# Kernel optimization log

Measured on AMD Instinct MI355X. Metric: run time of the kernel, lower is better.

Reference implementation:

```python
import jax, jax.numpy as jnp
import numpy as np

B, T, DIM = 2, 2048, 2048
N_HEADS, N_KV_HEADS = 32, 8
HEAD_DIM = DIM // N_HEADS          # 64
N_REP = N_HEADS // N_KV_HEADS      # 4
ROPE_THETA = 10000.0


def setup_inputs() -> dict:
    key = jax.random.key(0)
    ks = jax.random.split(key, 5)
    x = jax.random.normal(ks[0], (B, T, DIM), dtype=jnp.float32)
    # RoPE frequencies: freqs_cis[t, j] = exp(i * t * theta^{-2j/head_dim})
    inv_freq = 1.0 / (ROPE_THETA ** (jnp.arange(0, HEAD_DIM, 2, dtype=jnp.float32) / HEAD_DIM))
    angles = jnp.arange(T, dtype=jnp.float32)[:, None] * inv_freq[None, :]  # [T, HEAD_DIM//2]
    cos, sin = jnp.cos(angles), jnp.sin(angles)
    s = 0.02
    wq = jax.random.normal(ks[1], (N_HEADS * HEAD_DIM, DIM), dtype=jnp.float32) * s
    wk = jax.random.normal(ks[2], (N_KV_HEADS * HEAD_DIM, DIM), dtype=jnp.float32) * s
    wv = jax.random.normal(ks[3], (N_KV_HEADS * HEAD_DIM, DIM), dtype=jnp.float32) * s
    wo = jax.random.normal(ks[4], (DIM, DIM), dtype=jnp.float32) * s
    return {"x": x, "cos": cos, "sin": sin, "wq": wq, "wk": wk, "wv": wv, "wo": wo}


def _apply_rope(t, cos, sin):
    # t: [B, T, H, D]; cos/sin: [T, D//2]. Complex multiply on interleaved pairs.
    b, tt, h, d = t.shape
    tr = t.reshape(b, tt, h, d // 2, 2)
    t0, t1 = tr[..., 0], tr[..., 1]
    c = cos[None, :, None, :]
    s = sin[None, :, None, :]
    o0 = t0 * c - t1 * s
    o1 = t0 * s + t1 * c
    return jnp.stack([o0, o1], axis=-1).reshape(b, tt, h, d)


def reference(x, cos, sin, wq, wk, wv, wo):
    Bs, Ts, C = x.shape
    # Projections (nn.Linear, no bias): y = x @ W^T
    q = jnp.einsum('btc,oc->bto', x, wq).reshape(Bs, Ts, N_HEADS, HEAD_DIM)
    k = jnp.einsum('btc,oc->bto', x, wk).reshape(Bs, Ts, N_KV_HEADS, HEAD_DIM)
    v = jnp.einsum('btc,oc->bto', x, wv).reshape(Bs, Ts, N_KV_HEADS, HEAD_DIM)
    q = _apply_rope(q, cos[:Ts], sin[:Ts])
    k = _apply_rope(k, cos[:Ts], sin[:Ts])
    # [B, H, T, D]; GQA: broadcast kv heads via grouped einsum instead of repeat.
    q = q.transpose(0, 2, 1, 3).reshape(Bs, N_KV_HEADS, N_REP, Ts, HEAD_DIM)
    k = k.transpose(0, 2, 1, 3)  # [B, Hkv, T, D]
    v = v.transpose(0, 2, 1, 3)
    scale = 1.0 / jnp.sqrt(jnp.asarray(HEAD_DIM, dtype=x.dtype))
    scores = jnp.einsum('bgrqd,bgkd->bgrqk', q, k) * scale  # [B, Hkv, rep, T, T]
    causal = jnp.tril(jnp.ones((Ts, Ts), dtype=bool))
    scores = jnp.where(causal, scores, jnp.finfo(scores.dtype).min)
    attn = jax.nn.softmax(scores, axis=-1)
    y = jnp.einsum('bgrqk,bgkd->bgrqd', attn, v)           # [B, Hkv, rep, T, D]
    y = y.reshape(Bs, N_HEADS, Ts, HEAD_DIM).transpose(0, 2, 1, 3).reshape(Bs, Ts, C)
    return jnp.einsum('btc,oc->bto', y, wo)
```

## Files before the change

### kernel.cpp

```cpp
#include <hip/hip_runtime.h>

typedef __bf16 bf16;
typedef __attribute__((ext_vector_type(8))) __bf16 bf16x8;
typedef __attribute__((ext_vector_type(4))) __bf16 bf16x4;
typedef __attribute__((ext_vector_type(4))) float f32x4;

constexpr int T_SEQ = 2048;
constexpr int DIM   = 2048;
constexpr int NH    = 32;
constexpr int NKV   = 8;
constexpr int HD    = 64;
constexpr int QKV_N = DIM + 2 * NKV * HD;
constexpr int MROWS = 2 * T_SEQ;

__global__ void cast_all_kernel(const float* __restrict__ x,
                                const float* __restrict__ wq, const float* __restrict__ wk,
                                const float* __restrict__ wv, const float* __restrict__ wo,
                                bf16* __restrict__ xb, bf16* __restrict__ wqkv,
                                bf16* __restrict__ wob) {
  int stride = gridDim.x * blockDim.x;
  for (int g = blockIdx.x * blockDim.x + threadIdx.x; g < 4718592; g += stride) {
    const float* src; bf16* dst; int off;
    if (g < 2097152)      { src = x;  dst = xb;             off = g; }
    else if (g < 3145728) { src = wq; dst = wqkv;           off = g - 2097152; }
    else if (g < 3407872) { src = wk; dst = wqkv + 4194304; off = g - 3145728; }
    else if (g < 3670016) { src = wv; dst = wqkv + 5242880; off = g - 3407872; }
    else                  { src = wo; dst = wob;            off = g - 3670016; }
    float4 v = *(const float4*)(src + (size_t)off * 4);
    bf16x4 o = { (bf16)v.x, (bf16)v.y, (bf16)v.z, (bf16)v.w };
    *(bf16x4*)(dst + (size_t)off * 4) = o;
  }
}

template <typename OutT, bool ROPE>
__global__ __launch_bounds__(512) void gemm256(const bf16* __restrict__ A,
                                               const bf16* __restrict__ W,
                                               OutT* __restrict__ C,
                                               int N, int K, int cpx,
                                               const float* __restrict__ cs,
                                               const float* __restrict__ sn) {
  constexpr int BM = 256, BN = 128, BK = 64;
  __shared__ __attribute__((aligned(16))) bf16 Ab[3][BM * BK];
  __shared__ __attribute__((aligned(16))) bf16 Bb[3][BN * BK];
  const int tid = threadIdx.x, lane = tid & 63, wave = tid >> 6;
  const int l15 = lane & 15, l4 = lane >> 4;
  const int orig = blockIdx.x;
  const int wg = (orig & 7) * cpx + (orig >> 3);
  const int bm = (wg & 15) * BM;
  const int bn = (wg >> 4) * BN;
  const int wm = (wave >> 1) * 64, wn = (wave & 1) * 64;

  f32x4 acc[4][4] = {};

  const int NT = K / BK;
  auto stage = [&](int s, int k0) {
    #pragma unroll
    for (int i = 0; i < 4; ++i) {
      int c = i * 512 + tid;
      int row = c >> 3;
      int gc = ((c & 7) ^ (row & 7)) << 3;
      __builtin_amdgcn_global_load_lds(
          (const __attribute__((address_space(1))) unsigned int*)(A + (size_t)(bm + row) * K + k0 + gc),
          (__attribute__((address_space(3))) unsigned int*)(&Ab[s][0] + c * 8), 16, 0, 0);
    }
    #pragma unroll
    for (int i = 0; i < 2; ++i) {
      int c = i * 512 + tid;
      int row = c >> 3;
      int gc = ((c & 7) ^ (row & 7)) << 3;
      __builtin_amdgcn_global_load_lds(
          (const __attribute__((address_space(1))) unsigned int*)(W + (size_t)(bn + row) * K + k0 + gc),
          (__attribute__((address_space(3))) unsigned int*)(&Bb[s][0] + c * 8), 16, 0, 0);
    }
  };

  stage(0, 0);
  stage(1, BK);

  int d = 0;
  for (int t = 0; t < NT; ++t) {
    if (t + 1 < NT) { asm volatile("s_waitcnt vmcnt(6)" ::: "memory"); }
    else            { asm volatile("s_waitcnt vmcnt(0)" ::: "memory"); }
    __builtin_amdgcn_s_barrier();

    bf16x8 af[2][4], bfr[2][4];
    #pragma unroll
    for (int kk = 0; kk < 2; ++kk) {
      #pragma unroll
      for (int mi = 0; mi < 4; ++mi) {
        int row = wm + mi * 16 + l15;
        af[kk][mi] = *(const bf16x8*)((const char*)&Ab[d][0] + row * 128 +
                                      (((kk * 4 + l4) ^ (row & 7)) << 4));
      }
      #pragma unroll
      for (int ni = 0; ni < 4; ++ni) {
        int row = wn + ni * 16 + l15;
        bfr[kk][ni] = *(const bf16x8*)((const char*)&Bb[d][0] + row * 128 +
                                       (((kk * 4 + l4) ^ (row & 7)) << 4));
      }
    }

    if (t + 2 < NT) {
      int s = d + 2; if (s >= 3) s -= 3;
      stage(s, (t + 2) * BK);
    }

    __builtin_amdgcn_s_setprio(1);
    #pragma unroll
    for (int kk = 0; kk < 2; ++kk)
      #pragma unroll
      for (int mi = 0; mi < 4; ++mi)
        #pragma unroll
        for (int ni = 0; ni < 4; ++ni)
          acc[mi][ni] = __builtin_amdgcn_mfma_f32_16x16x32_bf16(af[kk][mi], bfr[kk][ni],
                                                                acc[mi][ni], 0, 0, 0);
    __builtin_amdgcn_s_setprio(0);

    ++d; if (d == 3) d = 0;
  }

  if constexpr (ROPE) {
    if (bn < 2560) {
      const bool odd = (l15 & 1);
      #pragma unroll
      for (int ni = 0; ni < 4; ++ni) {
        int col = bn + wn + ni * 16 + l15;
        int ip = (col & 63) >> 1;
        #pragma unroll
        for (int mi = 0; mi < 4; ++mi) {
          int row0 = wm + mi * 16 + l4 * 4;
          #pragma unroll
          for (int r = 0; r < 4; ++r) {
            int tpos = (bm + row0 + r) & (T_SEQ - 1);
            float c = cs[tpos * 32 + ip];
            float s = sn[tpos * 32 + ip];
            float a = acc[mi][ni][r];
            float p = __shfl_xor(a, 1);
            acc[mi][ni][r] = odd ? (p * s + a * c) : (a * c - p * s);
          }
        }
      }
    }
  }

  #pragma unroll
  for (int mi = 0; mi < 4; ++mi)
    #pragma unroll
    for (int ni = 0; ni < 4; ++ni) {
      size_t row = (size_t)bm + wm + mi * 16 + l4 * 4;
      int col = bn + wn + ni * 16 + l15;
      #pragma unroll
      for (int r = 0; r < 4; ++r)
        C[(row + r) * N + col] = (OutT)acc[mi][ni][r];
    }
}

__global__ __launch_bounds__(512, 2) void attn_kernel(const bf16* __restrict__ qkv,
                                                      bf16* __restrict__ y) {
  const int h = blockIdx.x, b = blockIdx.z;
  const int strip = 15 - blockIdx.y;
  const int g = h >> 2;
  const int tid = threadIdx.x, lane = tid & 63, wave = tid >> 6;
  const int l15 = lane & 15, l4 = lane >> 4;
  const int qbase = strip * 128 + wave * 16;

  __shared__ __attribute__((aligned(16))) bf16 Kb[2][128 * 64];
  __shared__ __attribute__((aligned(16))) bf16 VTs[2][2][64 * 64];
  __shared__ __attribute__((aligned(16))) bf16 Pb[8][16 * 64];

  constexpr float SCALE2 = 0.125f * 1.44269504088896f;
  constexpr float THR_RAW = 8.0f / SCALE2;
  constexpr int VOFF = DIM + NKV * HD;

  const bf16 one1 = (bf16)1.0f;
  const bf16x8 ones = { one1, one1, one1, one1, one1, one1, one1, one1 };

  bf16x8 qf[2];
  {
    const bf16* qp = qkv + ((size_t)b * T_SEQ + qbase + l15) * QKV_N + h * HD + l4 * 8;
    qf[0] = *(const bf16x8*)(qp);
    qf[1] = *(const bf16x8*)(qp + 32);
  }

  f32x4 oacc[4] = {};
  f32x4 lacc = {};
  float m_run = -INFINITY;
  const int qg = qbase + l15;

  const int nt = strip + 1;
  const size_t kvbase = (size_t)b * T_SEQ;
  const int vwoff = ((lane * 128 + wave * 16) ^ ((lane & 7) << 4));

  {
    #pragma unroll
    for (int i = 0; i < 2; ++i) {
      int chunk = i * 512 + tid;
      int row = chunk >> 3;
      int csrc = ((chunk & 7) << 3) ^ ((row & 7) << 3);
      __builtin_amdgcn_global_load_lds(
          (const __attribute__((address_space(1))) unsigned int*)
              (qkv + (kvbase + row) * QKV_N + DIM + g * HD + csrc),
          (__attribute__((address_space(3))) unsigned int*)(&Kb[0][0] + chunk * 8), 16, 0, 0);
    }
    #pragma unroll
    for (int hf = 0; hf < 2; ++hf) {
      const bf16* vp = qkv + (kvbase + hf * 64 + wave * 8) * QKV_N + VOFF + g * HD + lane;
      bf16x8 vr;
      #pragma unroll
      for (int j = 0; j < 8; ++j) vr[j] = vp[(size_t)j * QKV_N];
      *(bf16x8*)((char*)&VTs[0][hf][0] + vwoff) = vr;
    }
    asm volatile("s_waitcnt vmcnt(0)" ::: "memory");
    __syncthreads();
  }

  int cur = 0;
  for (int kt = 0; kt < nt; ++kt) {
    const bool has_next = (kt + 1) < nt;
    bf16x8 vr0, vr1;
    if (has_next) {
      #pragma unroll
      for (int i = 0; i < 2; ++i) {
        int chunk = i * 512 + tid;
        int row = chunk >> 3;
        int csrc = ((chunk & 7) << 3) ^ ((row & 7) << 3);
        __builtin_amdgcn_global_load_lds(
            (const __attribute__((address_space(1))) unsigned int*)
                (qkv + (kvbase + (kt + 1) * 128 + row) * QKV_N + DIM + g * HD + csrc),
            (__attribute__((address_space(3))) unsigned int*)(&Kb[cur ^ 1][0] + chunk * 8), 16, 0, 0);
      }
      const bf16* vp0 = qkv + (kvbase + (kt + 1) * 128 + wave * 8) * QKV_N + VOFF + g * HD + lane;
      const bf16* vp1 = vp0 + (size_t)64 * QKV_N;
      #pragma unroll
      for (int j = 0; j < 8; ++j) vr0[j] = vp0[(size_t)j * QKV_N];
      #pragma unroll
      for (int j = 0; j < 8; ++j) vr1[j] = vp1[(size_t)j * QKV_N];
    }

    const bf16* kb = &Kb[cur][0];
    const bool diag = (kt == strip);

    #pragma unroll
    for (int hf = 0; hf < 2; ++hf) {
      if (diag && hf == 1 && wave < 4) continue;

      f32x4 z[4];
      #pragma unroll
      for (int nt4 = 0; nt4 < 4; ++nt4) z[nt4] = (f32x4){0.f, 0.f, 0.f, 0.f};
      #pragma unroll
      for (int nt4 = 0; nt4 < 4; ++nt4)
        #pragma unroll
        for (int kk = 0; kk < 2; ++kk) {
          bf16x8 kf = *(const bf16x8*)((const char*)kb +
              (((hf * 64 + nt4 * 16 + l15) * 128 + (kk * 32 + l4 * 8) * 2) ^ ((l15 & 7) << 4)));
          z[nt4] = __builtin_amdgcn_mfma_f32_16x16x32_bf16(kf, qf[kk], z[nt4], 0, 0, 0);
        }

      if (diag) {
        #pragma unroll
        for (int nt4 = 0; nt4 < 4; ++nt4)
          #pragma unroll
          for (int r = 0; r < 4; ++r)
            if (kt * 128 + hf * 64 + nt4 * 16 + l4 * 4 + r > qg) z[nt4][r] = -INFINITY;
      }

      float a0 = fmaxf(fmaxf(z[0][0], z[0][1]), z[0][2]);
      float a1 = fmaxf(fmaxf(z[0][3], z[1][0]), z[1][1]);
      float a2 = fmaxf(fmaxf(z[1][2], z[1][3]), z[2][0]);
      float a3 = fmaxf(fmaxf(z[2][1], z[2][2]), z[2][3]);
      float a4 = fmaxf(fmaxf(z[3][0], z[3][1]), z[3][2]);
      float b0 = fmaxf(fmaxf(a0, a1), a2);
      float b1 = fmaxf(fmaxf(a3, a4), z[3][3]);
      float vm = fmaxf(b0, b1);
      vm = fmaxf(vm, __shfl_xor(vm, 16));
      vm = fmaxf(vm, __shfl_xor(vm, 32));

      if (!__all(vm - m_run <= THR_RAW)) {
        float mnew = fmaxf(m_run, vm);
        float alpha = __builtin_amdgcn_exp2f((m_run - mnew) * SCALE2);
        #pragma unroll
        for (int r = 0; r < 4; ++r) lacc[r] *= alpha;
        #pragma unroll
        for (int dt = 0; dt < 4; ++dt)
          #pragma unroll
          for (int r = 0; r < 4; ++r) oacc[dt][r] *= alpha;
        m_run = mnew;
      }
      const float ms = m_run * SCALE2;

      #pragma unroll
      for (int nt4 = 0; nt4 < 4; ++nt4)
        #pragma unroll
        for (int r = 0; r < 4; ++r)
          z[nt4][r] = __builtin_amdgcn_exp2f(__builtin_fmaf(z[nt4][r], SCALE2, -ms));

      bf16* pbw = &Pb[wave][0];
      #pragma unroll
      for (int nt4 = 0; nt4 < 4; ++nt4) {
        bf16x4 pk = { (bf16)z[nt4][0], (bf16)z[nt4][1], (bf16)z[nt4][2], (bf16)z[nt4][3] };
        *(bf16x4*)((char*)pbw + ((l15 * 128 + nt4 * 32 + l4 * 8) ^ ((l15 & 7) << 4))) = pk;
      }

      const bf16* vt = &VTs[cur][hf][0];
      #pragma unroll
      for (int kk = 0; kk < 2; ++kk) {
        bf16x8 pf = *(const bf16x8*)((const char*)pbw +
            ((l15 * 128 + kk * 64 + l4 * 16) ^ ((l15 & 7) << 4)));
        lacc = __builtin_amdgcn_mfma_f32_16x16x32_bf16(ones, pf, lacc, 0, 0, 0);
        #pragma unroll
        for (int dt = 0; dt < 4; ++dt) {
          bf16x8 vf = *(const bf16x8*)((const char*)vt +
              (((dt * 16 + l15) * 128 + (kk * 32 + l4 * 8) * 2) ^ ((l15 & 7) << 4)));
          oacc[dt] = __builtin_amdgcn_mfma_f32_16x16x32_bf16(vf, pf, oacc[dt], 0, 0, 0);
        }
      }
    }

    if (has_next) {
      *(bf16x8*)((char*)&VTs[cur ^ 1][0][0] + vwoff) = vr0;
      *(bf16x8*)((char*)&VTs[cur ^ 1][1][0] + vwoff) = vr1;
      __syncthreads();
      cur ^= 1;
    }
  }

  {
    float linv = __builtin_amdgcn_rcpf(lacc[0]);
    bf16* yp = y + ((size_t)b * T_SEQ + qbase + l15) * DIM + h * HD + l4 * 4;
    #pragma unroll
    for (int dt = 0; dt < 4; ++dt) {
      bf16x4 ov = { (bf16)(oacc[dt][0] * linv), (bf16)(oacc[dt][1] * linv),
                    (bf16)(oacc[dt][2] * linv), (bf16)(oacc[dt][3] * linv) };
      *(bf16x4*)(yp + dt * 16) = ov;
    }
  }
}

extern "C" void kernel_launch(void* const* d_in, const int* in_sizes, int n_in,
                              void* d_out, int out_size, void* d_ws, size_t ws_size,
                              hipStream_t stream) {
  const float* x    = (const float*)d_in[0];
  const float* cosb = (const float*)d_in[1];
  const float* sinb = (const float*)d_in[2];
  const float* wq   = (const float*)d_in[3];
  const float* wk   = (const float*)d_in[4];
  const float* wv   = (const float*)d_in[5];
  const float* wo   = (const float*)d_in[6];
  float* out = (float*)d_out;

  bf16* xb   = (bf16*)d_ws;
  bf16* wqkv = xb + (size_t)MROWS * DIM;
  bf16* wob  = wqkv + (size_t)QKV_N * DIM;
  bf16* qkv  = wob + (size_t)DIM * DIM;
  bf16* y    = qkv + (size_t)MROWS * QKV_N;

  cast_all_kernel<<<2048, 256, 0, stream>>>(x, wq, wk, wv, wo, xb, wqkv, wob);

  gemm256<bf16, true><<<384, 512, 0, stream>>>(xb, wqkv, qkv, QKV_N, DIM, 384 / 8, cosb, sinb);

  attn_kernel<<<dim3(NH, 16, 2), 512, 0, stream>>>(qkv, y);

  gemm256<float, false><<<256, 512, 0, stream>>>(y, wob, out, DIM, DIM, 256 / 8, nullptr, nullptr);
}
```

Measured before the change: 181.3 us.

## Use 256x192 tiles for QKV GEMM and rectangular block-to-tile mapping

New measurement: 164.4 us (median of 3 runs). 1.1x faster.

```diff
diff --git a/kernel.cpp b/kernel.cpp
--- a/kernel.cpp
+++ b/kernel.cpp
@@ -32,22 +32,24 @@
   }
 }
 
-template <typename OutT, bool ROPE>
+__device__ inline void rect_decode(int orig, int& bmi, int& bni) {
+  int c = orig & 7, i = orig >> 3;
+  bmi = (c & 1) * 8 + (i & 7);
+  bni = (c >> 1) * 4 + (i >> 3);
+}
+
 __global__ __launch_bounds__(512) void gemm256(const bf16* __restrict__ A,
                                                const bf16* __restrict__ W,
-                                               OutT* __restrict__ C,
-                                               int N, int K, int cpx,
-                                               const float* __restrict__ cs,
-                                               const float* __restrict__ sn) {
+                                               float* __restrict__ C,
+                                               int N, int K) {
   constexpr int BM = 256, BN = 128, BK = 64;
   __shared__ __attribute__((aligned(16))) bf16 Ab[3][BM * BK];
   __shared__ __attribute__((aligned(16))) bf16 Bb[3][BN * BK];
   const int tid = threadIdx.x, lane = tid & 63, wave = tid >> 6;
   const int l15 = lane & 15, l4 = lane >> 4;
-  const int orig = blockIdx.x;
-  const int wg = (orig & 7) * cpx + (orig >> 3);
-  const int bm = (wg & 15) * BM;
-  const int bn = (wg >> 4) * BN;
+  int bmi, bni;
+  rect_decode(blockIdx.x, bmi, bni);
+  const int bm = bmi * BM, bn = bni * BN;
   const int wm = (wave >> 1) * 64, wn = (wave & 1) * 64;
 
   f32x4 acc[4][4] = {};
@@ -119,30 +121,6 @@
     ++d; if (d == 3) d = 0;
   }
 
-  if constexpr (ROPE) {
-    if (bn < 2560) {
-      const bool odd = (l15 & 1);
-      #pragma unroll
-      for (int ni = 0; ni < 4; ++ni) {
-        int col = bn + wn + ni * 16 + l15;
-        int ip = (col & 63) >> 1;
-        #pragma unroll
-        for (int mi = 0; mi < 4; ++mi) {
-          int row0 = wm + mi * 16 + l4 * 4;
-          #pragma unroll
-          for (int r = 0; r < 4; ++r) {
-            int tpos = (bm + row0 + r) & (T_SEQ - 1);
-            float c = cs[tpos * 32 + ip];
-            float s = sn[tpos * 32 + ip];
-            float a = acc[mi][ni][r];
-            float p = __shfl_xor(a, 1);
-            acc[mi][ni][r] = odd ? (p * s + a * c) : (a * c - p * s);
-          }
-        }
-      }
-    }
-  }
-
   #pragma unroll
   for (int mi = 0; mi < 4; ++mi)
     #pragma unroll
@@ -151,7 +129,124 @@
       int col = bn + wn + ni * 16 + l15;
       #pragma unroll
       for (int r = 0; r < 4; ++r)
-        C[(row + r) * N + col] = (OutT)acc[mi][ni][r];
+        C[(row + r) * N + col] = acc[mi][ni][r];
+    }
+}
+
+__global__ __launch_bounds__(512, 1) void gemm192(const bf16* __restrict__ A,
+                                                  const bf16* __restrict__ W,
+                                                  bf16* __restrict__ C,
+                                                  const float* __restrict__ cs,
+                                                  const float* __restrict__ sn) {
+  constexpr int BM = 256, BN = 192, BK = 64, N = QKV_N, K = DIM;
+  __shared__ __attribute__((aligned(16))) bf16 Ab[3][BM * BK];
+  __shared__ __attribute__((aligned(16))) bf16 Bb[2][BN * BK];
+  const int tid = threadIdx.x, lane = tid & 63, wave = tid >> 6;
+  const int l15 = lane & 15, l4 = lane >> 4;
+  int bmi, bni;
+  rect_decode(blockIdx.x, bmi, bni);
+  const int bm = bmi * BM, bn = bni * BN;
+  const int wm = (wave >> 1) * 64, wn = (wave & 1) * 96;
+
+  f32x4 acc[4][6] = {};
+
+  constexpr int NT = K / BK;
+  auto stageA = [&](int s, int k0) {
+    #pragma unroll
+    for (int i = 0; i < 4; ++i) {
+      int c = i * 512 + tid;
+      int row = c >> 3;
+      int gc = ((c & 7) ^ (row & 7)) << 3;
+      __builtin_amdgcn_global_load_lds(
+          (const __attribute__((address_space(1))) unsigned int*)(A + (size_t)(bm + row) * K + k0 + gc),
+          (__attribute__((address_space(3))) unsigned int*)(&Ab[s][0] + c * 8), 16, 0, 0);
+    }
+  };
+  auto stageB = [&](int s, int k0) {
+    #pragma unroll
+    for (int i = 0; i < 3; ++i) {
+      int c = i * 512 + tid;
+      int row = c >> 3;
+      int gc = ((c & 7) ^ (row & 7)) << 3;
+      __builtin_amdgcn_global_load_lds(
+          (const __attribute__((address_space(1))) unsigned int*)(W + (size_t)(bn + row) * K + k0 + gc),
+          (__attribute__((address_space(3))) unsigned int*)(&Bb[s][0] + c * 8), 16, 0, 0);
+    }
+  };
+
+  stageA(0, 0);
+  stageB(0, 0);
+  stageA(1, BK);
+
+  for (int t = 0; t < NT; ++t) {
+    const int d3 = t % 3, db = t & 1;
+    if (t + 1 < NT) { asm volatile("s_waitcnt vmcnt(4)" ::: "memory"); }
+    else            { asm volatile("s_waitcnt vmcnt(0)" ::: "memory"); }
+    __builtin_amdgcn_s_barrier();
+
+    bf16x8 af[2][4], bfr[2][6];
+    #pragma unroll
+    for (int kk = 0; kk < 2; ++kk) {
+      #pragma unroll
+      for (int mi = 0; mi < 4; ++mi) {
+        int row = wm + mi * 16 + l15;
+        af[kk][mi] = *(const bf16x8*)((const char*)&Ab[d3][0] + row * 128 +
+                                      (((kk * 4 + l4) ^ (row & 7)) << 4));
+      }
+      #pragma unroll
+      for (int ni = 0; ni < 6; ++ni) {
+        int row = wn + ni * 16 + l15;
+        bfr[kk][ni] = *(const bf16x8*)((const char*)&Bb[db][0] + row * 128 +
+                                       (((kk * 4 + l4) ^ (row & 7)) << 4));
+      }
+    }
+
+    if (t + 1 < NT) stageB(db ^ 1, (t + 1) * BK);
+    if (t + 2 < NT) { int s = d3 + 2; if (s >= 3) s -= 3; stageA(s, (t + 2) * BK); }
+
+    __builtin_amdgcn_s_setprio(1);
+    #pragma unroll
+    for (int kk = 0; kk < 2; ++kk)
+      #pragma unroll
+      for (int mi = 0; mi < 4; ++mi)
+        #pragma unroll
+        for (int ni = 0; ni < 6; ++ni)
+          acc[mi][ni] = __builtin_amdgcn_mfma_f32_16x16x32_bf16(af[kk][mi], bfr[kk][ni],
+                                                                acc[mi][ni], 0, 0, 0);
+    __builtin_amdgcn_s_setprio(0);
+  }
+
+  const bool odd = (l15 & 1);
+  #pragma unroll
+  for (int ni = 0; ni < 6; ++ni) {
+    if (bn + wn + ni * 16 < 2560) {
+      int col = bn + wn + ni * 16 + l15;
+      int ip = (col & 63) >> 1;
+      #pragma unroll
+      for (int mi = 0; mi < 4; ++mi) {
+        int row0 = wm + mi * 16 + l4 * 4;
+        #pragma unroll
+        for (int r = 0; r < 4; ++r) {
+          int tpos = (bm + row0 + r) & (T_SEQ - 1);
+          float c = cs[tpos * 32 + ip];
+          float s = sn[tpos * 32 + ip];
+          float a = acc[mi][ni][r];
+          float p = __shfl_xor(a, 1);
+          acc[mi][ni][r] = odd ? (p * s + a * c) : (a * c - p * s);
+        }
+      }
+    }
+  }
+
+  #pragma unroll
+  for (int mi = 0; mi < 4; ++mi)
+    #pragma unroll
+    for (int ni = 0; ni < 6; ++ni) {
+      size_t row = (size_t)bm + wm + mi * 16 + l4 * 4;
+      int col = bn + wn + ni * 16 + l15;
+      #pragma unroll
+      for (int r = 0; r < 4; ++r)
+        C[(row + r) * N + col] = (bf16)acc[mi][ni][r];
     }
 }
 
@@ -356,9 +451,9 @@
 
   cast_all_kernel<<<2048, 256, 0, stream>>>(x, wq, wk, wv, wo, xb, wqkv, wob);
 
-  gemm256<bf16, true><<<384, 512, 0, stream>>>(xb, wqkv, qkv, QKV_N, DIM, 384 / 8, cosb, sinb);
+  gemm192<<<256, 512, 0, stream>>>(xb, wqkv, qkv, cosb, sinb);
 
   attn_kernel<<<dim3(NH, 16, 2), 512, 0, stream>>>(qkv, y);
 
-  gemm256<float, false><<<256, 512, 0, stream>>>(y, wob, out, DIM, DIM, 256 / 8, nullptr, nullptr);
-}
+  gemm256<<<256, 512, 0, stream>>>(y, wob, out, DIM, DIM);
+}
```
